# Performance work log

Measured on AMD Instinct MI355X. Metric: run time of the kernel, lower is better.

Reference implementation:

```python
import jax, jax.numpy as jnp
import numpy as np

EPS = 1e-5  # BatchNorm2d default eps


def _binarize_ste(x):
    """Forward: sign(x). Backward: hardtanh STE (grad 1 where |x|<=1, else 0)."""
    xc = jnp.clip(x, -1.0, 1.0)
    return xc + jax.lax.stop_gradient(jnp.sign(x) - xc)


def setup_inputs() -> dict:
    key = jax.random.key(0)
    k1, k2, k3, k4 = jax.random.split(key, 4)
    x = jax.random.normal(k1, (32, 256, 32, 32), dtype=jnp.float32)
    # BatchNorm affine params (affine=True)
    gamma = 1.0 + 0.1 * jax.random.normal(k2, (256,), dtype=jnp.float32)
    beta = 0.1 * jax.random.normal(k3, (256,), dtype=jnp.float32)
    # Conv weight, OIHW, bias=False
    W = 0.05 * jax.random.normal(k4, (256, 256, 3, 3), dtype=jnp.float32)
    return {"x": x, "gamma": gamma, "beta": beta, "W": W}


def reference(x, gamma, beta, W):
    # BatchNorm2d, training-mode batch statistics over (N, H, W) per channel
    mean = jnp.mean(x, axis=(0, 2, 3), keepdims=True)
    var = jnp.var(x, axis=(0, 2, 3), keepdims=True)
    xn = (x - mean) * jax.lax.rsqrt(var + EPS)
    xn = xn * gamma[None, :, None, None] + beta[None, :, None, None]
    # Conv2d_1w1a: binarize activations and weights (sign fwd / STE bwd), then conv
    a = _binarize_ste(xn)
    wb = _binarize_ste(W)
    out = jax.lax.conv_general_dilated(
        a, wb,
        window_strides=(1, 1),
        padding=((1, 1), (1, 1)),
        dimension_numbers=("NCHW", "OIHW", "NCHW"),
    )
    return out
```

## Files before the change

kernel.cpp:

```cpp
#include <hip/hip_runtime.h>
#include <hip/hip_bf16.h>


#define NIMG 32
#define C    256
#define K    256

typedef int v4i  __attribute__((ext_vector_type(4)));
typedef int v16i __attribute__((ext_vector_type(16)));

#define AHT_IMG 295936
#define AHT_KB  36992
#define AHT_ROW 1088


__global__ __launch_bounds__(256) void k_stats_packw(
    const float* __restrict__ x, const float* __restrict__ W,
    double2* __restrict__ partials, char* __restrict__ wfrag) {
  int bx = blockIdx.x;
  int tid = threadIdx.x;
  if (bx >= 2048) {
    int k = bx - 2048, c = tid;
    const float* src = W + ((size_t)k * 256 + c) * 9;
    char* dst = wfrag + (size_t)(c >> 4) * 4096 + k * 16 + (c & 15);
    #pragma unroll
    for (int t = 0; t < 9; ++t)
      dst[(size_t)t * 65536] = (src[t] > 0.0f) ? (char)1 : (char)-1;
    return;
  }
  int c = bx >> 3, grp = bx & 7;
  double s = 0.0, sq = 0.0;
  #pragma unroll
  for (int ni = 0; ni < 4; ++ni) {
    int n = grp * 4 + ni;
    const float* p = x + (size_t)n * (C * 1024) + (size_t)c * 1024;
    float4 v = ((const float4*)p)[tid];
    s += (double)v.x + (double)v.y + (double)v.z + (double)v.w;
    sq += (double)v.x * v.x + (double)v.y * v.y
        + (double)v.z * v.z + (double)v.w * v.w;
  }
  for (int o = 32; o > 0; o >>= 1) {
    s += __shfl_down(s, o);
    sq += __shfl_down(sq, o);
  }
  __shared__ double ls[4], lq[4];
  if ((tid & 63) == 0) { ls[tid >> 6] = s; lq[tid >> 6] = sq; }
  __syncthreads();
  if (tid == 0) {
    double2 r;
    r.x = ls[0] + ls[1] + ls[2] + ls[3];
    r.y = lq[0] + lq[1] + lq[2] + lq[3];
    partials[c * 8 + grp] = r;
  }
}

__global__ __launch_bounds__(256) void k_packa_i8(
    const float* __restrict__ x, const double2* __restrict__ partials,
    const float* __restrict__ gamma, const float* __restrict__ beta,
    char* __restrict__ aHT) {
  __shared__ float lf[32 * 257];
  __shared__ float lthr[256];
  __shared__ unsigned lfl[256];
  int y = blockIdx.x, n = blockIdx.y, tid = threadIdx.x;

  {
    double S = 0.0, Q = 0.0;
    #pragma unroll
    for (int g = 0; g < 8; ++g) {
      double2 p = partials[tid * 8 + g];
      S += p.x; Q += p.y;
    }
    const double N = 32768.0;
    double mean = S / N;
    double var = Q / N - mean * mean;
    double rs = 1.0 / sqrt(var + 1e-5);
    double gm = (double)gamma[tid];
    double bt = (double)beta[tid];
    float t;
    unsigned flip;
    if (gm == 0.0) {
      t = (bt > 0.0) ? -3.0e38f : 3.0e38f;
      flip = 0u;
    } else {
      t = (float)(mean - bt / (rs * gm));
      flip = (gm < 0.0) ? 1u : 0u;
    }
    lthr[tid] = t;
    lfl[tid] = flip;
  }

  #pragma unroll
  for (int it = 0; it < 8; ++it) {
    int c = it * 32 + (tid >> 3), q = tid & 7;
    float4 v = *(const float4*)(x + (size_t)n * 262144 + (size_t)c * 1024
                                + y * 32 + q * 4);
    lf[(q * 4 + 0) * 257 + c] = v.x;
    lf[(q * 4 + 1) * 257 + c] = v.y;
    lf[(q * 4 + 2) * 257 + c] = v.z;
    lf[(q * 4 + 3) * 257 + c] = v.w;
  }
  __syncthreads();
  int xl = tid & 31, cb = tid >> 5;
  unsigned wds[8];
  #pragma unroll
  for (int g = 0; g < 8; ++g) {
    unsigned wv = 0;
    #pragma unroll
    for (int jj = 0; jj < 4; ++jj) {
      int c = cb * 32 + g * 4 + jj;
      float v = lf[xl * 257 + c];
      unsigned bit = ((v > lthr[c]) ? 1u : 0u) ^ lfl[c];
      unsigned byte = bit ? 0x01u : 0xFFu;
      wv |= byte << (8 * jj);
    }
    wds[g] = wv;
  }
  char* dst = aHT + ((size_t)n * 8 + cb) * AHT_KB
            + (size_t)(y + 1) * AHT_ROW + (size_t)(xl + 1) * 32;
  uint4 u0, u1;
  u0.x = wds[0]; u0.y = wds[1]; u0.z = wds[2]; u0.w = wds[3];
  u1.x = wds[4]; u1.y = wds[5]; u1.z = wds[6]; u1.w = wds[7];
  *(uint4*)dst = u0;
  *((uint4*)dst + 1) = u1;

  uint4 z; z.x = 0; z.y = 0; z.z = 0; z.w = 0;
  if (xl < 2) {
    char* hz = aHT + ((size_t)n * 8 + cb) * AHT_KB
             + (size_t)(y + 1) * AHT_ROW + (size_t)(xl * 33) * 32;
    *(uint4*)hz = z;
    *((uint4*)hz + 1) = z;
  }
  if (y == 0 || y == 31) {
    int row = (y == 0) ? 0 : 33;
    for (int idx = tid; idx < 272; idx += 256) {
      int kb = idx / 34, xx = idx % 34;
      char* hz = aHT + ((size_t)n * 8 + kb) * AHT_KB
               + (size_t)row * AHT_ROW + (size_t)xx * 32;
      *(uint4*)hz = z;
      *((uint4*)hz + 1) = z;
    }
  }
}

__global__ __launch_bounds__(512) void k_conv_mfma(
    const char* __restrict__ aHT, const char* __restrict__ wfrag,
    float* __restrict__ out) {
  __shared__ uint4 As4[3264];
  char* As = (char*)As4;
  int tid = threadIdx.x;
  int lane = tid & 63, w = tid >> 6;
  int nh = w & 3, mb = w >> 2;
  int bx = blockIdx.x;
  int lb = (bx & 7) * 32 + (bx >> 3);
  int n = lb >> 3, ys = lb & 7;
  int y0 = ys * 4;
  int yw = y0 + mb * 2;
  int xl = lane & 31, hi = lane >> 5;

  {
    const char* aImg = aHT + (size_t)n * AHT_IMG;
    for (int e = tid; e < 3264; e += 512) {
      int px = e % 34;
      int q = e / 34;
      int hs = q & 1;
      int q2 = q >> 1;
      int rl = q2 % 6;
      int kb = q2 / 6;
      const char* g = aImg + (size_t)kb * AHT_KB
                    + (size_t)(y0 + rl) * AHT_ROW + px * 32 + hs * 16;
      *(v4i*)(As + (size_t)e * 16) = *(const v4i*)g;
    }
  }
  __syncthreads();

  const char* wB = wfrag + hi * 4096 + (nh * 64 + xl) * 16;
  int aBase = (mb * 2 + 1) * 1088 + hi * 544 + (xl + 1) * 16;

  v16i a00 = {0}, a01 = {0}, a10 = {0}, a11 = {0};
  v4i B[3][4];

  #define LOADB(P, S)                                                         \
    { const char* bp_ = wB + (size_t)(P) * 16384;                             \
      B[S][0] = *(const v4i*)(bp_);                                           \
      B[S][1] = *(const v4i*)(bp_ + 512);                                     \
      B[S][2] = *(const v4i*)(bp_ + 8192);                                    \
      B[S][3] = *(const v4i*)(bp_ + 8704); }

  LOADB(0, 0);
  LOADB(1, 1);
  LOADB(2, 2);

  #pragma unroll
  for (int p = 0; p < 36; ++p) {
    const int set = p % 3;
    int tap = p >> 2, kb0 = (p & 3) * 2;
    int dy = tap / 3 - 1, dx = tap % 3 - 1;
    int ab = aBase + kb0 * 6528 + dy * 1088 + dx * 16;
    v4i Ar0k0 = *(const v4i*)(As + ab);
    v4i Ar1k0 = *(const v4i*)(As + ab + 1088);
    v4i Ar0k1 = *(const v4i*)(As + ab + 6528);
    v4i Ar1k1 = *(const v4i*)(As + ab + 6528 + 1088);
    __builtin_amdgcn_s_setprio(1);
    a00 = __builtin_amdgcn_mfma_i32_32x32x32_i8(Ar0k0, B[set][0], a00, 0, 0, 0);
    a01 = __builtin_amdgcn_mfma_i32_32x32x32_i8(Ar0k0, B[set][1], a01, 0, 0, 0);
    a10 = __builtin_amdgcn_mfma_i32_32x32x32_i8(Ar1k0, B[set][0], a10, 0, 0, 0);
    a11 = __builtin_amdgcn_mfma_i32_32x32x32_i8(Ar1k0, B[set][1], a11, 0, 0, 0);
    a00 = __builtin_amdgcn_mfma_i32_32x32x32_i8(Ar0k1, B[set][2], a00, 0, 0, 0);
    a01 = __builtin_amdgcn_mfma_i32_32x32x32_i8(Ar0k1, B[set][3], a01, 0, 0, 0);
    a10 = __builtin_amdgcn_mfma_i32_32x32x32_i8(Ar1k1, B[set][2], a10, 0, 0, 0);
    a11 = __builtin_amdgcn_mfma_i32_32x32x32_i8(Ar1k1, B[set][3], a11, 0, 0, 0);
    __builtin_amdgcn_s_setprio(0);
    if (p < 33) LOADB(p + 3, set);
  }
  #undef LOADB

  size_t ob0 = (size_t)n * 262144 + (size_t)(nh * 64 + xl) * 1024
             + (size_t)yw * 32 + 4 * hi;
  #pragma unroll
  for (int r = 0; r < 2; ++r) {
    #pragma unroll
    for (int nb = 0; nb < 2; ++nb) {
      v16i av = (r == 0) ? (nb == 0 ? a00 : a01) : (nb == 0 ? a10 : a11);
      float* obp = out + ob0 + (size_t)nb * 32768 + r * 32;
      #pragma unroll
      for (int q = 0; q < 4; ++q) {
        float4 f;
        f.x = (float)av[q * 4 + 0];
        f.y = (float)av[q * 4 + 1];
        f.z = (float)av[q * 4 + 2];
        f.w = (float)av[q * 4 + 3];
        *(float4*)(obp + 8 * q) = f;
      }
    }
  }
}


__global__ __launch_bounds__(256) void k_stats_part_fb(
    const float* __restrict__ x, double2* __restrict__ partials) {
  int grp = blockIdx.x;
  int c = blockIdx.y;
  int tid = threadIdx.x;
  double s = 0.0, sq = 0.0;
  #pragma unroll
  for (int ni = 0; ni < 4; ++ni) {
    int n = grp * 4 + ni;
    const float* p = x + (size_t)n * (C * 1024) + (size_t)c * 1024;
    float4 v = ((const float4*)p)[tid];
    s += (double)v.x + (double)v.y + (double)v.z + (double)v.w;
    sq += (double)v.x * v.x + (double)v.y * v.y
        + (double)v.z * v.z + (double)v.w * v.w;
  }
  for (int o = 32; o > 0; o >>= 1) {
    s += __shfl_down(s, o);
    sq += __shfl_down(sq, o);
  }
  __shared__ double ls[4], lq[4];
  if ((tid & 63) == 0) { ls[tid >> 6] = s; lq[tid >> 6] = sq; }
  __syncthreads();
  if (tid == 0) {
    double2 r;
    r.x = ls[0] + ls[1] + ls[2] + ls[3];
    r.y = lq[0] + lq[1] + lq[2] + lq[3];
    partials[c * 8 + grp] = r;
  }
}

__global__ __launch_bounds__(256) void k_packw_corr_final(
    const float* __restrict__ W, const double2* __restrict__ partials,
    const float* __restrict__ gamma, const float* __restrict__ beta,
    unsigned* __restrict__ wp, int* __restrict__ corr,
    unsigned* __restrict__ zp, float* __restrict__ t_out,
    unsigned* __restrict__ flip_out) {
  int bk = blockIdx.x;
  int tid = threadIdx.x;
  if (bk == 256) {
    int c = tid;
    double S = 0.0, Q = 0.0;
    #pragma unroll
    for (int g = 0; g < 8; ++g) {
      double2 p = partials[c * 8 + g];
      S += p.x; Q += p.y;
    }
    const double N = 32768.0;
    double mean = S / N;
    double var = Q / N - mean * mean;
    double rs = 1.0 / sqrt(var + 1e-5);
    double g = (double)gamma[c];
    double b = (double)beta[c];
    float t;
    unsigned flip;
    if (g == 0.0) {
      t = (b > 0.0) ? -3.0e38f : 3.0e38f;
      flip = 0u;
    } else {
      t = (float)(mean - b / (rs * g));
      flip = (g < 0.0) ? 1u : 0u;
    }
    t_out[c] = t;
    flip_out[c] = flip;
    return;
  }
  int k = bk;
  __shared__ unsigned lw[72];
  float w[9];
  const float* src = W + (size_t)k * 2304 + (size_t)tid * 9;
  #pragma unroll
  for (int t = 0; t < 9; ++t) w[t] = src[t];
  int lane = tid & 63, wv = tid >> 6;
  #pragma unroll
  for (int t = 0; t < 9; ++t) {
    unsigned long long m = __ballot(w[t] > 0.0f);
    if (lane == 0) {
      lw[t * 8 + 2 * wv] = (unsigned)m;
      lw[t * 8 + 2 * wv + 1] = (unsigned)(m >> 32);
    }
  }
  __syncthreads();
  if (tid < 72) wp[(size_t)k * 72 + tid] = lw[tid];
  if (tid >= 128 && tid < 144) {
    int cls = tid - 128;
    int sum = 0;
    #pragma unroll
    for (int t = 0; t < 9; ++t) {
      int dy = t / 3 - 1, dx = t % 3 - 1;
      bool inv = (((cls & 1) && dx == -1) || ((cls & 2) && dx == 1) ||
                  ((cls & 4) && dy == -1) || ((cls & 8) && dy == 1));
      if (inv) {
        #pragma unroll
        for (int j = 0; j < 8; ++j) sum += __popc(lw[t * 8 + j]);
      }
    }
    corr[k * 16 + cls] = sum;
  }
  if (bk == 0 && tid >= 192 && tid < 200) zp[tid - 192] = 0u;
}

__global__ __launch_bounds__(256) void k_packa_bits(
    const float* __restrict__ x, const float* __restrict__ t,
    const unsigned* __restrict__ flip, unsigned* __restrict__ ap) {
  int n = blockIdx.y;
  int p0 = blockIdx.x * 64;
  int pix = threadIdx.x & 63;
  int q = threadIdx.x >> 6;
  unsigned w0 = 0, w1 = 0;
  const float* xb = x + (size_t)n * (C * 1024) + p0 + pix;
  #pragma unroll
  for (int i = 0; i < 64; ++i) {
    int c = q * 64 + i;
    float tv = t[c];
    unsigned fl = flip[c];
    float v = xb[(size_t)c * 1024];
    unsigned bit = ((v > tv) ? 1u : 0u) ^ fl;
    if (i < 32) w0 |= bit << i;
    else        w1 |= bit << (i - 32);
  }
  uint2 st; st.x = w0; st.y = w1;
  *(uint2*)(ap + ((size_t)n * 1024 + p0 + pix) * 8 + q * 2) = st;
}

__global__ __launch_bounds__(256) void k_conv_pop(
    const unsigned* __restrict__ ap, const unsigned* __restrict__ wp,
    const int* __restrict__ corr, const unsigned* __restrict__ zp,
    float* __restrict__ out) {
  int n = blockIdx.z;
  int ystrip = blockIdx.y;
  int kc = blockIdx.x;
  int tid = threadIdx.x;
  int lane = tid & 63;
  int wave = tid >> 6;
  int y = ystrip * 8 + wave * 2 + (lane >> 5);
  int xx = lane & 31;
  int cls = (xx == 0 ? 1 : 0) | (xx == 31 ? 2 : 0) |
            (y == 0 ? 4 : 0) | (y == 31 ? 8 : 0);
  uint4 a0[9], a1[9];
  int nv = 0;
  const uint4* zp4 = (const uint4*)zp;
  #pragma unroll
  for (int t = 0; t < 9; ++t) {
    int dy = t / 3 - 1, dx = t % 3 - 1;
    int cy = y + dy, cx = xx + dx;
    bool valid = (cy >= 0) & (cy < 32) & (cx >= 0) & (cx < 32);
    nv += valid ? 1 : 0;
    const uint4* pa = valid
        ? (const uint4*)(ap + (((size_t)n * 32 + cy) * 32 + cx) * 8)
        : zp4;
    a0[t] = pa[0];
    a1[t] = pa[1];
  }
  int bias = nv << 8;
  float* ob = out + (size_t)n * (K * 1024) + (size_t)y * 32 + xx;
  for (int kk = 0; kk < 16; ++kk) {
    int k = kc * 16 + kk;
    const uint4* wq = (const uint4*)(wp + (size_t)k * 72);
    int s0 = 0, s1 = 0, s2 = 0, s3 = 0, s4 = 0, s5 = 0, s6 = 0, s7 = 0;
    #pragma unroll
    for (int t = 0; t < 9; ++t) {
      uint4 wa = wq[t * 2];
      uint4 wb = wq[t * 2 + 1];
      s0 += __popc(a0[t].x ^ wa.x);
      s1 += __popc(a0[t].y ^ wa.y);
      s2 += __popc(a0[t].z ^ wa.z);
      s3 += __popc(a0[t].w ^ wa.w);
      s4 += __popc(a1[t].x ^ wb.x);
      s5 += __popc(a1[t].y ^ wb.y);
      s6 += __popc(a1[t].z ^ wb.z);
      s7 += __popc(a1[t].w ^ wb.w);
    }
    int S = ((s0 + s1) + (s2 + s3)) + ((s4 + s5) + (s6 + s7));
    int tot = corr[(k << 4) + cls] - S;
    ob[(size_t)k * 1024] = (float)(bias + 2 * tot);
  }
}


extern "C" void kernel_launch(void* const* d_in, const int* in_sizes, int n_in,
                              void* d_out, int out_size, void* d_ws, size_t ws_size,
                              hipStream_t stream) {
  const float* x = (const float*)d_in[0];
  const float* gamma = (const float*)d_in[1];
  const float* beta = (const float*)d_in[2];
  const float* W = (const float*)d_in[3];
  float* out = (float*)d_out;
  char* ws = (char*)d_ws;

  const size_t NEED = 655360 + (size_t)NIMG * AHT_IMG;
  if (ws_size >= NEED) {
    double2* partials = (double2*)(ws + 4096);
    char* wfrag = ws + 36864;
    char* aHT = ws + 655360;

    k_stats_packw<<<2304, 256, 0, stream>>>(x, W, partials, wfrag);
    k_packa_i8<<<dim3(32, 32), 256, 0, stream>>>(x, partials, gamma, beta, aHT);
    k_conv_mfma<<<256, 512, 0, stream>>>(aHT, wfrag, out);
  } else {
    float* t = (float*)ws;
    unsigned* flip = (unsigned*)(ws + 1024);
    unsigned* wp = (unsigned*)(ws + 4096);
    unsigned* zp = (unsigned*)(ws + 77824);
    int* corr = (int*)(ws + 78336);
    double2* partials = (double2*)(ws + 98304);
    unsigned* ap = (unsigned*)(ws + 131072);

    k_stats_part_fb<<<dim3(8, 256), 256, 0, stream>>>(x, partials);
    k_packw_corr_final<<<257, 256, 0, stream>>>(W, partials, gamma, beta,
                                                wp, corr, zp, t, flip);
    k_packa_bits<<<dim3(16, 32), 256, 0, stream>>>(x, t, flip, ap);
    k_conv_pop<<<dim3(16, 4, 32), 256, 0, stream>>>(ap, wp, corr, zp, out);
  }
}
```

Before: 48.19 us.

## Split conv output channels across two blocks to double grid size

The MFMA conv kernel now launches 512 blocks instead of 256, each covering half of the 256 output channels, with every wave computing a 32x(2 rows) tile instead of 64x(2 rows). This gives more blocks on the 256-CU part and reduces accumulator and B register pressure, with a launch-bounds hint for higher occupancy. The cost is that each block still loads the full activation tile into LDS, so activation global and LDS traffic doubles, and each wave reuses each A fragment less.

```diff
diff --git a/kernel.cpp b/kernel.cpp
--- a/kernel.cpp
+++ b/kernel.cpp
@@ -142,19 +142,18 @@
   }
 }
 
-__global__ __launch_bounds__(512) void k_conv_mfma(
+__global__ __launch_bounds__(512, 4) void k_conv_mfma(
     const char* __restrict__ aHT, const char* __restrict__ wfrag,
     float* __restrict__ out) {
   __shared__ uint4 As4[3264];
   char* As = (char*)As4;
   int tid = threadIdx.x;
   int lane = tid & 63, w = tid >> 6;
-  int nh = w & 3, mb = w >> 2;
+  int rp = w >> 2, nt = w & 3;
   int bx = blockIdx.x;
-  int lb = (bx & 7) * 32 + (bx >> 3);
-  int n = lb >> 3, ys = lb & 7;
+  int lb = (bx & 7) * 64 + (bx >> 3);
+  int n = lb >> 4, ys = (lb >> 1) & 7, kh = lb & 1;
   int y0 = ys * 4;
-  int yw = y0 + mb * 2;
   int xl = lane & 31, hi = lane >> 5;
 
   {
@@ -173,18 +172,16 @@
   }
   __syncthreads();
 
-  const char* wB = wfrag + hi * 4096 + (nh * 64 + xl) * 16;
-  int aBase = (mb * 2 + 1) * 1088 + hi * 544 + (xl + 1) * 16;
-
-  v16i a00 = {0}, a01 = {0}, a10 = {0}, a11 = {0};
-  v4i B[3][4];
+  const char* wB = wfrag + hi * 4096 + (kh * 128 + nt * 32 + xl) * 16;
+  int aBase = (rp * 2 + 1) * 1088 + hi * 544 + (xl + 1) * 16;
+
+  v16i a0 = {0}, a1 = {0};
+  v4i B[3][2];
 
   #define LOADB(P, S)                                                         \
     { const char* bp_ = wB + (size_t)(P) * 16384;                             \
       B[S][0] = *(const v4i*)(bp_);                                           \
-      B[S][1] = *(const v4i*)(bp_ + 512);                                     \
-      B[S][2] = *(const v4i*)(bp_ + 8192);                                    \
-      B[S][3] = *(const v4i*)(bp_ + 8704); }
+      B[S][1] = *(const v4i*)(bp_ + 8192); }
 
   LOADB(0, 0);
   LOADB(1, 1);
@@ -201,36 +198,29 @@
     v4i Ar0k1 = *(const v4i*)(As + ab + 6528);
     v4i Ar1k1 = *(const v4i*)(As + ab + 6528 + 1088);
     __builtin_amdgcn_s_setprio(1);
-    a00 = __builtin_amdgcn_mfma_i32_32x32x32_i8(Ar0k0, B[set][0], a00, 0, 0, 0);
-    a01 = __builtin_amdgcn_mfma_i32_32x32x32_i8(Ar0k0, B[set][1], a01, 0, 0, 0);
-    a10 = __builtin_amdgcn_mfma_i32_32x32x32_i8(Ar1k0, B[set][0], a10, 0, 0, 0);
-    a11 = __builtin_amdgcn_mfma_i32_32x32x32_i8(Ar1k0, B[set][1], a11, 0, 0, 0);
-    a00 = __builtin_amdgcn_mfma_i32_32x32x32_i8(Ar0k1, B[set][2], a00, 0, 0, 0);
-    a01 = __builtin_amdgcn_mfma_i32_32x32x32_i8(Ar0k1, B[set][3], a01, 0, 0, 0);
-    a10 = __builtin_amdgcn_mfma_i32_32x32x32_i8(Ar1k1, B[set][2], a10, 0, 0, 0);
-    a11 = __builtin_amdgcn_mfma_i32_32x32x32_i8(Ar1k1, B[set][3], a11, 0, 0, 0);
+    a0 = __builtin_amdgcn_mfma_i32_32x32x32_i8(Ar0k0, B[set][0], a0, 0, 0, 0);
+    a1 = __builtin_amdgcn_mfma_i32_32x32x32_i8(Ar1k0, B[set][0], a1, 0, 0, 0);
+    a0 = __builtin_amdgcn_mfma_i32_32x32x32_i8(Ar0k1, B[set][1], a0, 0, 0, 0);
+    a1 = __builtin_amdgcn_mfma_i32_32x32x32_i8(Ar1k1, B[set][1], a1, 0, 0, 0);
     __builtin_amdgcn_s_setprio(0);
     if (p < 33) LOADB(p + 3, set);
   }
   #undef LOADB
 
-  size_t ob0 = (size_t)n * 262144 + (size_t)(nh * 64 + xl) * 1024
-             + (size_t)yw * 32 + 4 * hi;
+  size_t ob0 = (size_t)n * 262144 + (size_t)(kh * 128 + nt * 32 + xl) * 1024
+             + (size_t)(y0 + rp * 2) * 32 + 4 * hi;
   #pragma unroll
   for (int r = 0; r < 2; ++r) {
-    #pragma unroll
-    for (int nb = 0; nb < 2; ++nb) {
-      v16i av = (r == 0) ? (nb == 0 ? a00 : a01) : (nb == 0 ? a10 : a11);
-      float* obp = out + ob0 + (size_t)nb * 32768 + r * 32;
-      #pragma unroll
-      for (int q = 0; q < 4; ++q) {
-        float4 f;
-        f.x = (float)av[q * 4 + 0];
-        f.y = (float)av[q * 4 + 1];
-        f.z = (float)av[q * 4 + 2];
-        f.w = (float)av[q * 4 + 3];
-        *(float4*)(obp + 8 * q) = f;
-      }
+    v16i av = (r == 0) ? a0 : a1;
+    float* obp = out + ob0 + (size_t)r * 32;
+    #pragma unroll
+    for (int q = 0; q < 4; ++q) {
+      float4 f;
+      f.x = (float)av[q * 4 + 0];
+      f.y = (float)av[q * 4 + 1];
+      f.z = (float)av[q * 4 + 2];
+      f.w = (float)av[q * 4 + 3];
+      *(float4*)(obp + 8 * q) = f;
     }
   }
 }
@@ -432,7 +422,7 @@
 
     k_stats_packw<<<2304, 256, 0, stream>>>(x, W, partials, wfrag);
     k_packa_i8<<<dim3(32, 32), 256, 0, stream>>>(x, partials, gamma, beta, aHT);
-    k_conv_mfma<<<256, 512, 0, stream>>>(aHT, wfrag, out);
+    k_conv_mfma<<<512, 512, 0, stream>>>(aHT, wfrag, out);
   } else {
     float* t = (float*)ws;
     unsigned* flip = (unsigned*)(ws + 1024);
```

Result: slower. 70.16 us (+45.6%).
